# Optimization experiments

Measured on AMD Instinct MI355X. Metric: run time of the kernel, lower is better.

## Reference

```python
import jax, jax.numpy as jnp
import numpy as np

BN_EPS = 1e-5
LRELU_SLOPE = 0.1
F = 512  # feature dim fixed by ReFineBlock/Fc_ClassBlock input_dim


def _bn_eval(x, gamma, beta, mean, var):
    # BatchNorm1d in eval mode (running stats); elementwise over feature dim
    return (x - mean) * (gamma / jnp.sqrt(var + BN_EPS)) + beta


def _lrelu(x):
    return jnp.where(x > 0, x, LRELU_SLOPE * x)


def setup_inputs() -> dict:
    key = jax.random.key(0)
    ks = jax.random.split(key, 16)
    B, P, G = 128, 1, 4
    d = jax.random.normal(ks[0], (B, B, P, G, F), dtype=jnp.float32)
    w = jax.random.uniform(ks[1], (B * G, B * G), dtype=jnp.float32)
    W1 = jax.random.normal(ks[2], (F, F), dtype=jnp.float32) * 0.04
    b1 = jnp.zeros((F,), dtype=jnp.float32)
    g1 = jnp.ones((F,), dtype=jnp.float32)
    beta1 = jnp.zeros((F,), dtype=jnp.float32)
    m1 = jax.random.normal(ks[3], (F,), dtype=jnp.float32) * 0.1
    v1 = jax.random.uniform(ks[4], (F,), jnp.float32, 0.5, 1.5)
    W2 = jax.random.normal(ks[5], (F, F), dtype=jnp.float32) * 0.04
    b2 = jnp.zeros((F,), dtype=jnp.float32)
    g2 = jnp.ones((F,), dtype=jnp.float32)
    beta2 = jnp.zeros((F,), dtype=jnp.float32)
    m2 = jax.random.normal(ks[6], (F,), dtype=jnp.float32) * 0.1
    v2 = jax.random.uniform(ks[7], (F,), jnp.float32, 0.5, 1.5)
    # Fc_ClassBlock.classifier: Dropout(eval=id) + Linear(512, 2)
    Wc = jax.random.normal(ks[8], (2, F), dtype=jnp.float32) * 0.001
    bc = jnp.zeros((2,), dtype=jnp.float32)
    return {"d": d, "w": w, "W1": W1, "b1": b1, "g1": g1, "beta1": beta1,
            "m1": m1, "v1": v1, "W2": W2, "b2": b2, "g2": g2, "beta2": beta2,
            "m2": m2, "v2": v2, "Wc": Wc, "bc": bc}


def reference(d, w, W1, b1, g1, beta1, m1, v1, W2, b2, g2, beta2, m2, v2, Wc, bc):
    batch_size = d.shape[1]          # len(d[0])
    num_g = d.shape[3]
    feat = d.shape[-1]
    N = batch_size * num_g           # adjacency size

    # Vectorized ReFineBlock over every (k, :, i, j) row (eval mode: dropout=id)
    x = d.reshape(-1, feat)
    h = _lrelu(_bn_eval(x @ W1.T + b1, g1, beta1, m1, v1))
    h = _lrelu(_bn_eval(h @ W2.T + b2, g2, beta2, m2, v2))
    t = h.reshape(batch_size, -1, feat)   # (B, B*G, F)

    # preprocess_adj: adj = w + I; D^{-1/2}; (adj @ D).T @ D
    adj = w.reshape(N, N) + jnp.eye(N, dtype=w.dtype)
    rowsum = adj.sum(axis=1)
    d_inv_sqrt = jnp.power(rowsum, -0.5)
    d_inv_sqrt = jnp.where(jnp.isinf(d_inv_sqrt), 0.0, d_inv_sqrt)
    w_norm = (adj * d_inv_sqrt[None, :]).T * d_inv_sqrt[None, :]  # (N, N)

    # GCN propagation: d_new[:, :, i] = t[:, :, i] @ w_norm for each feature i
    d_new = jnp.einsum('bmf,mn->bnf', t, w_norm)  # (B, N, F)

    # classifier.classifier (dropout=id + Linear) applied per probe row
    result = d_new @ Wc.T + bc  # (B, N, 2)
    return result.reshape(-1, 2)
```

## Files before the change

### kernel.cpp

```cpp
#include <hip/hip_runtime.h>
#include <hip/hip_bf16.h>


typedef __hip_bfloat16 bf16_t;
typedef __bf16 bf16x8 __attribute__((ext_vector_type(8)));
typedef __bf16 bf16x4 __attribute__((ext_vector_type(4)));
typedef float f32x4 __attribute__((ext_vector_type(4)));

#define KDIM 512
#define BM 64

__device__ __forceinline__ void gload_lds16(const void* g, void* l) {
    __builtin_amdgcn_global_load_lds(
        (const __attribute__((address_space(1))) unsigned int*)g,
        (__attribute__((address_space(3))) unsigned int*)l,
        16, 0, 0);
}

__device__ __forceinline__ float ldsel(const void* p, int i, int isbf) {
    return isbf ? __bfloat162float(((const bf16_t*)p)[i]) : ((const float*)p)[i];
}

__global__ void probe_kernel(const void* __restrict__ d, int* __restrict__ flag) {
    const unsigned short* u = (const unsigned short*)d;
    const int l = threadIdx.x;
    int cnt = 0;
    for (int i = l; i < 256; i += 64) {
        const int e = (u[i] >> 7) & 0xFF;
        cnt += (e >= 118 && e <= 129) ? 1 : 0;
    }
    #pragma unroll
    for (int off = 32; off; off >>= 1) cnt += __shfl_down(cnt, off, 64);
    if (l == 0) *flag = (cnt >= 200) ? 1 : 0;
}

__global__ void rowsum_kernel(const void* __restrict__ w, const int* __restrict__ flagp,
                              float* __restrict__ dinv) {
    const int isbf = *flagp;
    const int i = blockIdx.x;
    const int l = threadIdx.x;
    float s = 0.f;
    for (int j = l; j < 512; j += 64) s += ldsel(w, i * 512 + j, isbf);
    #pragma unroll
    for (int off = 32; off; off >>= 1) s += __shfl_down(s, off, 64);
    if (l == 0) dinv[i] = 1.0f / sqrtf(s + 1.0f);
}

__global__ void params_kernel(const void* g1, const void* b1, const void* m1,
                              const void* v1, const void* be1,
                              const void* g2, const void* b2, const void* m2,
                              const void* v2, const void* be2,
                              const void* Wc, const void* bc,
                              const int* __restrict__ flagp,
                              float* sc1, float* sh1, float* sc2, float* sh2,
                              float* wcf, float* bcf) {
    const int isbf = *flagp;
    const int i = threadIdx.x;
    float s1 = ldsel(g1, i, isbf) / sqrtf(ldsel(v1, i, isbf) + 1e-5f);
    sc1[i] = s1;
    sh1[i] = (ldsel(b1, i, isbf) - ldsel(m1, i, isbf)) * s1 + ldsel(be1, i, isbf);
    float s2 = ldsel(g2, i, isbf) / sqrtf(ldsel(v2, i, isbf) + 1e-5f);
    sc2[i] = s2;
    sh2[i] = (ldsel(b2, i, isbf) - ldsel(m2, i, isbf)) * s2 + ldsel(be2, i, isbf);
    wcf[i] = ldsel(Wc, i, isbf);
    wcf[512 + i] = ldsel(Wc, 512 + i, isbf);
    if (i < 2) bcf[i] = ldsel(bc, i, isbf);
}

__global__ void wconv_kernel(const void* __restrict__ W1, const void* __restrict__ W2,
                             const int* __restrict__ flagp,
                             bf16_t* __restrict__ W1pk, bf16_t* __restrict__ W2pk) {
    const int isbf = *flagp;
    const int t = blockIdx.x * 256 + threadIdx.x;
    const int lane = t & 63;
    const int kt = (t >> 6) & 15;
    const int c16 = t >> 10;
    const int src = (c16 * 16 + (lane & 15)) * 512 + kt * 32 + (lane >> 4) * 8;
    bf16x8 v1, v2;
    #pragma unroll
    for (int e = 0; e < 8; ++e) {
        v1[e] = (__bf16)ldsel(W1, src + e, isbf);
        v2[e] = (__bf16)ldsel(W2, src + e, isbf);
    }
    *reinterpret_cast<bf16x8*>(W1pk + (size_t)t * 8) = v1;
    *reinterpret_cast<bf16x8*>(W2pk + (size_t)t * 8) = v2;
}

__global__ void wnorm_kernel(const void* __restrict__ w, const int* __restrict__ flagp,
                             const float* __restrict__ dinv, float* __restrict__ wn_t) {
    const int isbf = *flagp;
    const int idx = blockIdx.x * 256 + threadIdx.x;
    const int n = idx >> 9, m = idx & 511;
    float a = ldsel(w, n * 512 + m, isbf) + (m == n ? 1.0f : 0.0f);
    wn_t[idx] = a * dinv[m] * dinv[n];
}

#define FJSTRIDE 16384
#define FKSTRIDE 1024

#define LOADW4(dst, base, kt)                                                  \
    _Pragma("unroll")                                                          \
    for (int j_ = 0; j_ < 4; ++j_)                                             \
        dst[j_] = *reinterpret_cast<const bf16x8*>((base) + j_ * FJSTRIDE + (kt) * FKSTRIDE);

#define STAGE(kt, buf)                                                         \
    {                                                                          \
        if (isbf) {                                                            \
            const bf16_t* sp_ = (const bf16_t*)A + sgb + (size_t)(kt) * 32;    \
            bf16x4 b4_ = *reinterpret_cast<const bf16x4*>(sp_);                \
            f32x4 f_;                                                          \
            f_.x = (float)b4_[0]; f_.y = (float)b4_[1];                        \
            f_.z = (float)b4_[2]; f_.w = (float)b4_[3];                        \
            *reinterpret_cast<f32x4*>((char*)AsgF + (buf) * 8192 + tid * 16) = f_; \
        } else {                                                               \
            gload_lds16((const char*)A + (sgb + (size_t)(kt) * 32) * 4,        \
                        (char*)AsgF + (buf) * 8192 + wave * 1024);             \
        }                                                                      \
    }

#define COMPUTE(kt, buf, bWs)                                                  \
    _Pragma("unroll")                                                          \
    for (int i_ = 0; i_ < 4; ++i_) {                                           \
        const int r_ = i_ * 16 + rl;                                           \
        const int rb_ = (buf) * 8192 + r_ * 128;                               \
        const int s_ = r_ & 7;                                                 \
        f32x4 q0_ = *reinterpret_cast<const f32x4*>(                           \
            (const char*)AsgF + rb_ + (((2 * hi) ^ s_) << 4));                 \
        f32x4 q1_ = *reinterpret_cast<const f32x4*>(                           \
            (const char*)AsgF + rb_ + (((2 * hi + 1) ^ s_) << 4));             \
        bf16x8 af_;                                                            \
        af_[0]=(__bf16)q0_.x; af_[1]=(__bf16)q0_.y; af_[2]=(__bf16)q0_.z; af_[3]=(__bf16)q0_.w; \
        af_[4]=(__bf16)q1_.x; af_[5]=(__bf16)q1_.y; af_[6]=(__bf16)q1_.z; af_[7]=(__bf16)q1_.w; \
        _Pragma("unroll")                                                      \
        for (int j_ = 0; j_ < 4; ++j_)                                         \
            acc[j_][i_] = __builtin_amdgcn_mfma_f32_16x16x32_bf16(bWs[j_], af_, acc[j_][i_], 0, 0, 0); \
    }

#define COMPT1(kt, bWs)                                                        \
    _Pragma("unroll")                                                          \
    for (int i_ = 0; i_ < 4; ++i_) {                                           \
        const int row_ = i_ * 16 + rl;                                         \
        int off_ = (row_ << 10) + (kt) * 64 + hi * 16;                         \
        off_ ^= (row_ & 7) << 4;                                               \
        bf16x8 af_ = *reinterpret_cast<const bf16x8*>((const char*)T1s + off_);\
        _Pragma("unroll")                                                      \
        for (int j_ = 0; j_ < 4; ++j_)                                         \
            acc[j_][i_] = __builtin_amdgcn_mfma_f32_16x16x32_bf16(bWs[j_], af_, acc[j_][i_], 0, 0, 0); \
    }

__launch_bounds__(512, 4)
__global__ void fused_mlp(const void* __restrict__ A,
                          const bf16_t* __restrict__ W1pk,
                          const bf16_t* __restrict__ W2pk,
                          const float* __restrict__ sc1, const float* __restrict__ sh1,
                          const float* __restrict__ sc2, const float* __restrict__ sh2,
                          const float* __restrict__ wcf,
                          const int* __restrict__ flagp,
                          float* __restrict__ U)
{
    __shared__ __align__(16) bf16_t T1s[BM * KDIM];
    __shared__ __align__(16) float AsgF[2][BM * 32];
    float* UredF = (float*)AsgF;

    const int isbf = *flagp;
    const int tid = threadIdx.x;
    const int wave = tid >> 6, lane = tid & 63;
    const int rl = lane & 15, hi = lane >> 4;
    const int wc = wave;
    const int tile = blockIdx.x;

    const char* w1base = (const char*)W1pk + ((size_t)(wc * 4) * 16 * 64 + lane) * 16;
    const char* w2base = (const char*)W2pk + ((size_t)(wc * 4) * 16 * 64 + lane) * 16;

    const int srow = tid >> 3;
    const int schk = (tid & 7) ^ (srow & 7);
    const size_t sgb = ((size_t)(tile * BM) + srow) * KDIM + schk * 4;

    f32x4 acc[4][4] = {};

    STAGE(0, 0);
    __syncthreads();

    {
        bf16x8 bW[4];
        #pragma unroll 1
        for (int kt = 0; kt < 16; ++kt) {
            if (kt + 1 < 16) STAGE(kt + 1, (kt + 1) & 1);
            LOADW4(bW, w1base, kt);
            COMPUTE(kt, kt & 1, bW);
            __syncthreads();
        }
    }

    #pragma unroll
    for (int j = 0; j < 4; ++j) {
        const int col0 = wc * 64 + j * 16 + hi * 4;
        const f32x4 s4 = *reinterpret_cast<const f32x4*>(&sc1[col0]);
        const f32x4 h4 = *reinterpret_cast<const f32x4*>(&sh1[col0]);
        #pragma unroll
        for (int i = 0; i < 4; ++i) {
            const int row = i * 16 + rl;
            int off = (row << 10) + (col0 << 1);
            off ^= (row & 7) << 4;
            bf16x4 pk;
            #pragma unroll
            for (int r = 0; r < 4; ++r) {
                float y = acc[j][i][r] * s4[r] + h4[r];
                y = y > 0.f ? y : 0.1f * y;
                pk[r] = (__bf16)y;
            }
            *reinterpret_cast<bf16x4*>((char*)T1s + off) = pk;
        }
    }
    __syncthreads();

    #pragma unroll
    for (int j = 0; j < 4; ++j)
        #pragma unroll
        for (int i = 0; i < 4; ++i)
            acc[j][i] = f32x4{0.f, 0.f, 0.f, 0.f};

    {
        bf16x8 bW0[4], bW1[4];
        LOADW4(bW0, w2base, 0);
        #pragma unroll 1
        for (int kt = 0; kt < 16; kt += 2) {
            LOADW4(bW1, w2base, kt + 1);
            COMPT1(kt, bW0);
            if (kt + 2 < 16) LOADW4(bW0, w2base, kt + 2);
            COMPT1(kt + 1, bW1);
        }
    }

    float p0[4] = {0.f, 0.f, 0.f, 0.f}, p1[4] = {0.f, 0.f, 0.f, 0.f};
    #pragma unroll
    for (int j = 0; j < 4; ++j) {
        const int col0 = wc * 64 + j * 16 + hi * 4;
        const f32x4 s4 = *reinterpret_cast<const f32x4*>(&sc2[col0]);
        const f32x4 h4 = *reinterpret_cast<const f32x4*>(&sh2[col0]);
        const f32x4 w0 = *reinterpret_cast<const f32x4*>(&wcf[col0]);
        const f32x4 w1 = *reinterpret_cast<const f32x4*>(&wcf[512 + col0]);
        #pragma unroll
        for (int i = 0; i < 4; ++i)
            #pragma unroll
            for (int r = 0; r < 4; ++r) {
                float y = acc[j][i][r] * s4[r] + h4[r];
                y = y > 0.f ? y : 0.1f * y;
                p0[i] += y * w0[r];
                p1[i] += y * w1[r];
            }
    }
    #pragma unroll
    for (int i = 0; i < 4; ++i) {
        float a = p0[i], b = p1[i];
        a += __shfl_xor(a, 16, 64);  b += __shfl_xor(b, 16, 64);
        a += __shfl_xor(a, 32, 64);  b += __shfl_xor(b, 32, 64);
        if (hi == 0) {
            UredF[(wc * BM + i * 16 + rl) * 2]     = a;
            UredF[(wc * BM + i * 16 + rl) * 2 + 1] = b;
        }
    }
    __syncthreads();
    if (tid < BM * 2) {
        const int row = tid >> 1, c = tid & 1;
        float s = 0.f;
        #pragma unroll
        for (int q = 0; q < 8; ++q) s += UredF[(q * BM + row) * 2 + c];
        U[(size_t)(tile * BM + row) * 2 + c] = s;
    }
}

__global__ void gcn_kernel(const float* __restrict__ wn_t, const float* __restrict__ U,
                           const float* __restrict__ bcf, const int* __restrict__ flagp,
                           void* __restrict__ out) {
    const int isbf = *flagp;
    const int wave = threadIdx.x >> 6, lane = threadIdx.x & 63;
    const int task = blockIdx.x * 4 + wave;
    const int b = task >> 9, n = task & 511;
    const float* wrow = wn_t + n * 512;
    const float* ub = U + b * 1024;
    float a0 = 0.f, a1 = 0.f;
    for (int m = lane; m < 512; m += 64) {
        const float wv = wrow[m];
        a0 += wv * ub[m * 2];
        a1 += wv * ub[m * 2 + 1];
    }
    #pragma unroll
    for (int off = 32; off; off >>= 1) {
        a0 += __shfl_down(a0, off, 64);
        a1 += __shfl_down(a1, off, 64);
    }
    if (lane == 0) {
        const float r0 = a0 + bcf[0];
        const float r1 = a1 + bcf[1];
        if (isbf) {
            ((bf16_t*)out)[task * 2]     = __float2bfloat16(r0);
            ((bf16_t*)out)[task * 2 + 1] = __float2bfloat16(r1);
        } else {
            ((float*)out)[task * 2]     = r0;
            ((float*)out)[task * 2 + 1] = r1;
        }
    }
}

extern "C" void kernel_launch(void* const* d_in, const int* in_sizes, int n_in,
                              void* d_out, int out_size, void* d_ws, size_t ws_size,
                              hipStream_t stream) {
    const void* d   = d_in[0];
    const void* w   = d_in[1];
    const void* W1  = d_in[2];
    const void* b1  = d_in[3];
    const void* g1  = d_in[4];
    const void* be1 = d_in[5];
    const void* m1  = d_in[6];
    const void* v1  = d_in[7];
    const void* W2  = d_in[8];
    const void* b2  = d_in[9];
    const void* g2  = d_in[10];
    const void* be2 = d_in[11];
    const void* m2  = d_in[12];
    const void* v2  = d_in[13];
    const void* Wc  = d_in[14];
    const void* bc  = d_in[15];

    char* ws = (char*)d_ws;
    float*  wn_t = (float*)ws;
    bf16_t* W1pk = (bf16_t*)(ws + 0x100000);
    bf16_t* W2pk = (bf16_t*)(ws + 0x180000);
    float*  sc1  = (float*)(ws + 0x200000);
    float*  sh1  = sc1 + 512;
    float*  sc2  = sh1 + 512;
    float*  sh2  = sc2 + 512;
    float*  dinv = sh2 + 512;
    float*  wcf  = (float*)(ws + 0x204000);
    float*  bcf  = (float*)(ws + 0x205000);
    int*    flag = (int*)(ws + 0x205100);
    float*  U    = (float*)(ws + 0x208000);

    const int M = 128 * 512;

    probe_kernel<<<1, 64, 0, stream>>>(d, flag);
    rowsum_kernel<<<512, 64, 0, stream>>>(w, flag, dinv);
    params_kernel<<<1, 512, 0, stream>>>(g1, b1, m1, v1, be1, g2, b2, m2, v2, be2,
                                         Wc, bc, flag, sc1, sh1, sc2, sh2, wcf, bcf);
    wconv_kernel<<<128, 256, 0, stream>>>(W1, W2, flag, W1pk, W2pk);
    wnorm_kernel<<<1024, 256, 0, stream>>>(w, flag, dinv, wn_t);

    fused_mlp<<<M / BM, 512, 0, stream>>>(d, W1pk, W2pk,
                                          sc1, sh1, sc2, sh2, wcf, flag, U);

    gcn_kernel<<<M / 4, 256, 0, stream>>>(wn_t, U, bcf, flag, d_out);
}
```

Before: 128.7 us.

## Stage activations into LDS as pre-converted bf16 fragments with register prefetch

Replaces the global->LDS direct fp32 staging (32-wide k tiles) with register-prefetched 64-wide k tiles that are converted to bf16 once and written to LDS in an MFMA-fragment layout. The compute loop then does a single 16-byte LDS read per fragment instead of two fp32 reads plus eight conversions, and the loop is unrolled into two double-buffered halves. It also adds a barrier before reusing the staging buffer for the reduction. The cost is more registers held for the prefetch and a conversion per element during staging.

```diff
diff --git a/kernel.cpp b/kernel.cpp
--- a/kernel.cpp
+++ b/kernel.cpp
@@ -9,13 +9,6 @@
 
 #define KDIM 512
 #define BM 64
-
-__device__ __forceinline__ void gload_lds16(const void* g, void* l) {
-    __builtin_amdgcn_global_load_lds(
-        (const __attribute__((address_space(1))) unsigned int*)g,
-        (__attribute__((address_space(3))) unsigned int*)l,
-        16, 0, 0);
-}
 
 __device__ __forceinline__ float ldsel(const void* p, int i, int isbf) {
     return isbf ? __bfloat162float(((const bf16_t*)p)[i]) : ((const float*)p)[i];
@@ -103,34 +96,34 @@
     for (int j_ = 0; j_ < 4; ++j_)                                             \
         dst[j_] = *reinterpret_cast<const bf16x8*>((base) + j_ * FJSTRIDE + (kt) * FKSTRIDE);
 
-#define STAGE(kt, buf)                                                         \
+#define SLOAD(S, r)                                                            \
     {                                                                          \
         if (isbf) {                                                            \
-            const bf16_t* sp_ = (const bf16_t*)A + sgb + (size_t)(kt) * 32;    \
-            bf16x4 b4_ = *reinterpret_cast<const bf16x4*>(sp_);                \
-            f32x4 f_;                                                          \
-            f_.x = (float)b4_[0]; f_.y = (float)b4_[1];                        \
-            f_.z = (float)b4_[2]; f_.w = (float)b4_[3];                        \
-            *reinterpret_cast<f32x4*>((char*)AsgF + (buf) * 8192 + tid * 16) = f_; \
+            sb##S = *reinterpret_cast<const bf16x8*>((const bf16_t*)A + sgb + (size_t)(r) * 64); \
         } else {                                                               \
-            gload_lds16((const char*)A + (sgb + (size_t)(kt) * 32) * 4,        \
-                        (char*)AsgF + (buf) * 8192 + wave * 1024);             \
+            const f32x4* p_ = (const f32x4*)((const float*)A + sgb + (size_t)(r) * 64); \
+            sf##S[0] = p_[0]; sf##S[1] = p_[1];                                \
         }                                                                      \
     }
 
-#define COMPUTE(kt, buf, bWs)                                                  \
+#define SWRITE(S, buf)                                                         \
+    {                                                                          \
+        bf16x8 v_;                                                             \
+        if (isbf) { v_ = sb##S; }                                              \
+        else {                                                                 \
+            v_[0] = (__bf16)sf##S[0].x; v_[1] = (__bf16)sf##S[0].y;            \
+            v_[2] = (__bf16)sf##S[0].z; v_[3] = (__bf16)sf##S[0].w;            \
+            v_[4] = (__bf16)sf##S[1].x; v_[5] = (__bf16)sf##S[1].y;            \
+            v_[6] = (__bf16)sf##S[1].z; v_[7] = (__bf16)sf##S[1].w;            \
+        }                                                                      \
+        *reinterpret_cast<bf16x8*>((char*)Asg + (buf) * 8192 + sldsoff) = v_;  \
+    }
+
+#define COMPUTEQ(buf, q, bWs)                                                  \
     _Pragma("unroll")                                                          \
     for (int i_ = 0; i_ < 4; ++i_) {                                           \
-        const int r_ = i_ * 16 + rl;                                           \
-        const int rb_ = (buf) * 8192 + r_ * 128;                               \
-        const int s_ = r_ & 7;                                                 \
-        f32x4 q0_ = *reinterpret_cast<const f32x4*>(                           \
-            (const char*)AsgF + rb_ + (((2 * hi) ^ s_) << 4));                 \
-        f32x4 q1_ = *reinterpret_cast<const f32x4*>(                           \
-            (const char*)AsgF + rb_ + (((2 * hi + 1) ^ s_) << 4));             \
-        bf16x8 af_;                                                            \
-        af_[0]=(__bf16)q0_.x; af_[1]=(__bf16)q0_.y; af_[2]=(__bf16)q0_.z; af_[3]=(__bf16)q0_.w; \
-        af_[4]=(__bf16)q1_.x; af_[5]=(__bf16)q1_.y; af_[6]=(__bf16)q1_.z; af_[7]=(__bf16)q1_.w; \
+        bf16x8 af_ = *reinterpret_cast<const bf16x8*>(                         \
+            (const char*)Asg + (buf) * 8192 + (q) * 4096 + i_ * 1024 + lane * 16); \
         _Pragma("unroll")                                                      \
         for (int j_ = 0; j_ < 4; ++j_)                                         \
             acc[j_][i_] = __builtin_amdgcn_mfma_f32_16x16x32_bf16(bWs[j_], af_, acc[j_][i_], 0, 0, 0); \
@@ -159,8 +152,8 @@
                           float* __restrict__ U)
 {
     __shared__ __align__(16) bf16_t T1s[BM * KDIM];
-    __shared__ __align__(16) float AsgF[2][BM * 32];
-    float* UredF = (float*)AsgF;
+    __shared__ __align__(16) bf16_t Asg[2][BM * 64];
+    float* UredF = (float*)Asg;
 
     const int isbf = *flagp;
     const int tid = threadIdx.x;
@@ -173,21 +166,37 @@
     const char* w2base = (const char*)W2pk + ((size_t)(wc * 4) * 16 * 64 + lane) * 16;
 
     const int srow = tid >> 3;
-    const int schk = (tid & 7) ^ (srow & 7);
-    const size_t sgb = ((size_t)(tile * BM) + srow) * KDIM + schk * 4;
+    const int sk8 = tid & 7;
+    const int sq = sk8 >> 2, sc8 = sk8 & 3;
+    const size_t sgb = ((size_t)(tile * BM) + srow) * KDIM + sk8 * 8;
+    const int sldsoff = (sq * 256 + (srow >> 4) * 64 + (srow & 15) + sc8 * 16) * 16;
 
     f32x4 acc[4][4] = {};
-
-    STAGE(0, 0);
+    f32x4 sfA[2], sfB[2];
+    bf16x8 sbA, sbB;
+
+    SLOAD(A, 0);
+    SWRITE(A, 0);
+    SLOAD(B, 1);
     __syncthreads();
 
     {
         bf16x8 bW[4];
         #pragma unroll 1
-        for (int kt = 0; kt < 16; ++kt) {
-            if (kt + 1 < 16) STAGE(kt + 1, (kt + 1) & 1);
-            LOADW4(bW, w1base, kt);
-            COMPUTE(kt, kt & 1, bW);
+        for (int r = 0; r < 8; r += 2) {
+            LOADW4(bW, w1base, 2 * r);
+            COMPUTEQ(0, 0, bW);
+            LOADW4(bW, w1base, 2 * r + 1);
+            COMPUTEQ(0, 1, bW);
+            SWRITE(B, 1);
+            if (r + 2 < 8) SLOAD(A, r + 2);
+            __syncthreads();
+            LOADW4(bW, w1base, 2 * r + 2);
+            COMPUTEQ(1, 0, bW);
+            LOADW4(bW, w1base, 2 * r + 3);
+            COMPUTEQ(1, 1, bW);
+            if (r + 2 < 8) SWRITE(A, 0);
+            if (r + 3 < 8) SLOAD(B, r + 3);
             __syncthreads();
         }
     }
@@ -250,6 +259,7 @@
                 p1[i] += y * w1[r];
             }
     }
+    __syncthreads();
     #pragma unroll
     for (int i = 0; i < 4; ++i) {
         float a = p0[i], b = p1[i];
```

Measured after the change: 180.2 us. 1.4x slower.
